# Performance work log

Measured on AMD Instinct MI355X. Metric: run time of the kernel, lower is better.

## Reference

```python
import jax, jax.numpy as jnp
import numpy as np

B = 8192
HID = 1024
VD = 1024
NH = 16
DH = HID // NH  # 64
TOPK = 8
LN_EPS = 1e-5


def setup_inputs() -> dict:
    key = jax.random.key(0)
    ks = jax.random.split(key, 10)
    s = 1.0 / np.sqrt(HID)
    return {
        "hidden_state": jax.random.normal(ks[0], (B, HID), dtype=jnp.float32),
        "memory_keys": jax.random.normal(ks[1], (B, TOPK, HID), dtype=jnp.float32),
        "memory_values": jax.random.normal(ks[2], (B, TOPK, VD), dtype=jnp.float32),
        "Wq": jax.random.normal(ks[3], (HID, HID), dtype=jnp.float32) * s,
        "Wk": jax.random.normal(ks[4], (HID, HID), dtype=jnp.float32) * s,
        "Wv": jax.random.normal(ks[5], (VD, HID), dtype=jnp.float32) * s,
        "Wo": jax.random.normal(ks[6], (HID, HID), dtype=jnp.float32) * s,
        "Wg": jax.random.normal(ks[7], (2 * HID, HID), dtype=jnp.float32) * s,
        "bg": jnp.zeros((HID,), dtype=jnp.float32),
        "ln_g": jnp.ones((HID,), dtype=jnp.float32),
        "ln_b": jnp.zeros((HID,), dtype=jnp.float32),
    }


def reference(hidden_state, memory_keys, memory_values, Wq, Wk, Wv, Wo, Wg, bg, ln_g, ln_b):
    b = hidden_state.shape[0]
    scale = DH ** -0.5
    # QKV projections, reshaped into heads
    Q = (hidden_state @ Wq).reshape(b, NH, DH)          # (B, H, D)
    K = (memory_keys @ Wk).reshape(b, TOPK, NH, DH)     # (B, K, H, D)
    V = (memory_values @ Wv).reshape(b, TOPK, NH, DH)   # (B, K, H, D)
    # attention over top_k memory slots (query length 1)
    scores = jnp.einsum("bhd,bkhd->bhk", Q, K) * scale  # (B, H, K)
    attn = jax.nn.softmax(scores, axis=-1)
    out = jnp.einsum("bhk,bkhd->bhd", attn, V).reshape(b, HID)
    memory_out = out @ Wo
    # gated residual
    gate_in = jnp.concatenate([hidden_state, memory_out], axis=-1)
    g = jax.nn.sigmoid(gate_in @ Wg + bg)
    aug = hidden_state + g * memory_out
    # LayerNorm (affine, eps=1e-5)
    mean = jnp.mean(aug, axis=-1, keepdims=True)
    var = jnp.var(aug, axis=-1, keepdims=True)
    return (aug - mean) * jax.lax.rsqrt(var + LN_EPS) * ln_g + ln_b
```

## Files before the change

kernel.cpp:

```cpp
#include <hip/hip_runtime.h>
#include <hip/hip_bf16.h>

typedef __bf16 bf16;
typedef __bf16 bf16x8 __attribute__((ext_vector_type(8)));
typedef __bf16 bf16x4 __attribute__((ext_vector_type(4)));
typedef float  f32x4  __attribute__((ext_vector_type(4)));

__device__ __forceinline__ void block_barrier()
{
    asm volatile("s_waitcnt lgkmcnt(0)\n\ts_barrier" ::: "memory");
}

#if defined(__has_builtin)
#if __has_builtin(__builtin_amdgcn_global_load_lds)
#define HAS_GLD 1
#endif
#endif
#ifndef HAS_GLD
#define HAS_GLD 0
#endif

__device__ __forceinline__ void gld_lds16(const bf16* g, bf16* lds_base)
{
#if HAS_GLD
    __builtin_amdgcn_global_load_lds(
        (const __attribute__((address_space(1))) void*)g,
        (__attribute__((address_space(3))) void*)lds_base, 16, 0, 0);
#else
    *(bf16x8*)(lds_base + (threadIdx.x & 63) * 8) = *(const bf16x8*)g;
#endif
}

__global__ __launch_bounds__(256)
void transpose_cvt(const float* __restrict__ src, bf16* __restrict__ dst, int K, int N)
{
    __shared__ float t[32][33];
    const int bx = blockIdx.x, by = blockIdx.y, tid = threadIdx.x;
    const int c = tid & 31, r0 = tid >> 5;
#pragma unroll
    for (int p = 0; p < 4; p++) {
        int r = r0 + p * 8;
        t[r][c] = src[(size_t)(by * 32 + r) * N + bx * 32 + c];
    }
    __syncthreads();
#pragma unroll
    for (int p = 0; p < 4; p++) {
        int r = r0 + p * 8;
        dst[(size_t)(bx * 32 + r) * K + by * 32 + c] = (bf16)t[c][r];
    }
}

__global__ __launch_bounds__(256)
void cvt_bf16(const float* __restrict__ src, bf16* __restrict__ dst, int n8)
{
    const int i = blockIdx.x * 256 + threadIdx.x;
    if (i >= n8) return;
    const float4* s = (const float4*)(src + (size_t)i * 8);
    float4 a = s[0], b = s[1];
    bf16x8 o;
    o[0] = (bf16)a.x; o[1] = (bf16)a.y; o[2] = (bf16)a.z; o[3] = (bf16)a.w;
    o[4] = (bf16)b.x; o[5] = (bf16)b.y; o[6] = (bf16)b.z; o[7] = (bf16)b.w;
    *(bf16x8*)(dst + (size_t)i * 8) = o;
}

__global__ __launch_bounds__(256)
void repack_wv(const bf16* __restrict__ Wvt, bf16* __restrict__ Wvf)
{
    const int t = blockIdx.x * 256 + threadIdx.x;
    const int lane = t & 63, g = t >> 6;
    const int dt = g & 3, sp = (g >> 2) & 31, h = g >> 7;
    const int lm = lane & 15, q = lane >> 4;
    const bf16x8 v = *(const bf16x8*)(Wvt + (size_t)(h * 64 + dt * 16 + lm) * 1024
                                      + sp * 32 + q * 8);
    *(bf16x8*)(Wvf + (size_t)g * 512 + lane * 8) = v;
}

template<bool TWOA>
__global__ __launch_bounds__(256)
void gemm_a97(const bf16* __restrict__ A1, const bf16* __restrict__ A2,
              const bf16* __restrict__ Bt, float* __restrict__ Cf,
              bf16* __restrict__ Cb, int Kloop, int Ksplit,
              int ldA, int ldA2, int ldB, int ldC,
              long az, long bz, long cz)
{
    __shared__ bf16 Al[128 * 32];
    __shared__ bf16 Bl[128 * 32];

    const int z = blockIdx.z;
    A1 += (size_t)z * az;
    Bt += (size_t)z * bz;
    if (Cf) Cf += (size_t)z * cz;
    if (Cb) Cb += (size_t)z * cz;

    int bx, by;
    {
        const int gy = gridDim.y;
        const int flat = blockIdx.y * gridDim.x + blockIdx.x;
        if ((gy & 7) == 0 && gridDim.x == 8) {
            const int xcd = flat & 7, slot = flat >> 3, mpx = gy >> 3;
            by = xcd * mpx + (slot >> 3);
            bx = slot & 7;
        } else { bx = blockIdx.x; by = blockIdx.y; }
    }

    const int tid = threadIdx.x;
    const int wave = tid >> 6, lane = tid & 63;
    const int m0 = by * 128, n0 = bx * 128;
    const int rl = lane >> 2;
    const int kc = (lane & 3) * 8;
    const int wm = wave >> 1, wn = wave & 1, lm = lane & 15, quad = lane >> 4;

    f32x4 acc[4][4];
#pragma unroll
    for (int i = 0; i < 4; i++)
#pragma unroll
        for (int j = 0; j < 4; j++)
#pragma unroll
            for (int r = 0; r < 4; r++) acc[i][j][r] = 0.f;

    for (int k0 = 0; k0 < Kloop; k0 += 32) {
        const bf16* Ab; int kof, ld;
        if (TWOA && k0 >= Ksplit) { Ab = A2; kof = k0 - Ksplit; ld = ldA2; }
        else                      { Ab = A1; kof = k0;          ld = ldA;  }
        const int r0 = wave * 32 + rl, r1 = r0 + 16;
        gld_lds16(Ab + (size_t)(m0 + r0) * ld + kof + kc, Al + (wave * 32) * 32);
        gld_lds16(Ab + (size_t)(m0 + r1) * ld + kof + kc, Al + (wave * 32 + 16) * 32);
        gld_lds16(Bt + (size_t)(n0 + r0) * ldB + k0 + kc, Bl + (wave * 32) * 32);
        gld_lds16(Bt + (size_t)(n0 + r1) * ldB + k0 + kc, Bl + (wave * 32 + 16) * 32);
        __syncthreads();

        bf16x8 af[4], bfr[4];
#pragma unroll
        for (int i = 0; i < 4; i++)
            af[i] = *(const bf16x8*)&Al[(wm * 64 + i * 16 + lm) * 32 + quad * 8];
#pragma unroll
        for (int j = 0; j < 4; j++)
            bfr[j] = *(const bf16x8*)&Bl[(wn * 64 + j * 16 + lm) * 32 + quad * 8];
#pragma unroll
        for (int i = 0; i < 4; i++)
#pragma unroll
            for (int j = 0; j < 4; j++)
                acc[i][j] = __builtin_amdgcn_mfma_f32_16x16x32_bf16(af[i], bfr[j], acc[i][j], 0, 0, 0);
        __syncthreads();
    }

#pragma unroll
    for (int i = 0; i < 4; i++) {
        const int rbase = m0 + wm * 64 + i * 16 + quad * 4;
#pragma unroll
        for (int j = 0; j < 4; j++) {
            const int c = n0 + wn * 64 + j * 16 + lm;
#pragma unroll
            for (int r = 0; r < 4; r++) {
                const float v = acc[i][j][r];
                const size_t idx = (size_t)(rbase + r) * ldC + c;
                if (Cf) Cf[idx] = v;
                if (Cb) Cb[idx] = (bf16)v;
            }
        }
    }
}

__global__ __launch_bounds__(512, 4)
void score_attn_part(const bf16* __restrict__ Qb, const bf16* __restrict__ Wkb,
                     const float* __restrict__ mk, float* __restrict__ part)
{
    __shared__ bf16 Ul[16 * 1024];

    const int tid  = threadIdx.x;
    const int wave = tid >> 6, lane = tid & 63;
    const int lm = lane & 15, q = lane >> 4;
    const int g  = blockIdx.x;
    const int c  = blockIdx.y;
    const int i0 = c * 64;
    const int h0 = wave * 2;

    bf16x8 wk[2][4][2];
#pragma unroll
    for (int hh = 0; hh < 2; hh++)
#pragma unroll
        for (int mt = 0; mt < 4; mt++) {
            const bf16* wp = Wkb + (size_t)(i0 + mt * 16 + lm) * 1024 + (h0 + hh) * 64 + q * 8;
            wk[hh][mt][0] = *(const bf16x8*)(wp);
            wk[hh][mt][1] = *(const bf16x8*)(wp + 32);
        }

    float* pbase = part + ((size_t)c << 20);

    for (int t = 0; t < 8; ++t) {
        const int b0 = g * 128 + t * 16;

        bf16x8 qf[2][2];
#pragma unroll
        for (int hh = 0; hh < 2; hh++) {
            const bf16* qp = Qb + (size_t)(b0 + lm) * 1024 + (h0 + hh) * 64 + q * 8;
            qf[hh][0] = *(const bf16x8*)(qp);
            qf[hh][1] = *(const bf16x8*)(qp + 32);
        }

#pragma unroll
        for (int hh = 0; hh < 2; hh++) {
            const int h = h0 + hh;
#pragma unroll
            for (int mt = 0; mt < 4; mt++) {
                f32x4 c4;
                c4[0] = 0.f; c4[1] = 0.f; c4[2] = 0.f; c4[3] = 0.f;
                c4 = __builtin_amdgcn_mfma_f32_16x16x32_bf16(wk[hh][mt][0], qf[hh][0], c4, 0, 0, 0);
                c4 = __builtin_amdgcn_mfma_f32_16x16x32_bf16(wk[hh][mt][1], qf[hh][1], c4, 0, 0, 0);
                bf16x4 o;
                o[0] = (bf16)c4[0]; o[1] = (bf16)c4[1]; o[2] = (bf16)c4[2]; o[3] = (bf16)c4[3];
                *(bf16x4*)((char*)Ul + ((((lm * 16 + h) * 64 + mt * 16 + q * 4) * 2)
                                        ^ (((lm ^ h) & 7) << 4))) = o;
            }
        }
        __syncthreads();

#pragma unroll
        for (int lb = 0; lb < 2; lb++) {
            const int bb = wave * 2 + lb;
            const float* mp = mk + (size_t)(b0 + bb) * 8192 + (lm & 7) * 1024 + i0 + q * 8;
            const f32x4 a0 = *(const f32x4*)(mp);
            const f32x4 a1 = *(const f32x4*)(mp + 4);
            const f32x4 b0v = *(const f32x4*)(mp + 32);
            const f32x4 b1v = *(const f32x4*)(mp + 36);
            bf16x8 m0, m1;
            m0[0] = (bf16)a0[0]; m0[1] = (bf16)a0[1]; m0[2] = (bf16)a0[2]; m0[3] = (bf16)a0[3];
            m0[4] = (bf16)a1[0]; m0[5] = (bf16)a1[1]; m0[6] = (bf16)a1[2]; m0[7] = (bf16)a1[3];
            m1[0] = (bf16)b0v[0]; m1[1] = (bf16)b0v[1]; m1[2] = (bf16)b0v[2]; m1[3] = (bf16)b0v[3];
            m1[4] = (bf16)b1v[0]; m1[5] = (bf16)b1v[1]; m1[6] = (bf16)b1v[2]; m1[7] = (bf16)b1v[3];

            const bf16x8 ua0 = *(const bf16x8*)((char*)Ul +
                ((((bb * 16 + lm) * 64 + q * 8) * 2) ^ (((bb ^ lm) & 7) << 4)));
            const bf16x8 ua1 = *(const bf16x8*)((char*)Ul +
                ((((bb * 16 + lm) * 64 + 32 + q * 8) * 2) ^ (((bb ^ lm) & 7) << 4)));

            f32x4 s4;
            s4[0] = 0.f; s4[1] = 0.f; s4[2] = 0.f; s4[3] = 0.f;
            s4 = __builtin_amdgcn_mfma_f32_16x16x32_bf16(ua0, m0, s4, 0, 0, 0);
            s4 = __builtin_amdgcn_mfma_f32_16x16x32_bf16(ua1, m1, s4, 0, 0, 0);

            if (lm < 8) {
                float* pp = pbase + (size_t)(b0 + bb) * 128 + lm;
#pragma unroll
                for (int r = 0; r < 4; r++) pp[(q * 4 + r) * 8] = s4[r];
            }
        }
        __syncthreads();
    }
}

__global__ __launch_bounds__(256)
void reduce_softmax(const float* __restrict__ part, float* __restrict__ attn)
{
    const int t = blockIdx.x * 256 + threadIdx.x;
    const float* p = part + (size_t)t * 8;
    float s[8] = {0.f, 0.f, 0.f, 0.f, 0.f, 0.f, 0.f, 0.f};
#pragma unroll
    for (int c = 0; c < 16; ++c) {
        const f32x4 a = *(const f32x4*)(p + ((size_t)c << 20));
        const f32x4 b = *(const f32x4*)(p + ((size_t)c << 20) + 4);
        s[0] += a[0]; s[1] += a[1]; s[2] += a[2]; s[3] += a[3];
        s[4] += b[0]; s[5] += b[1]; s[6] += b[2]; s[7] += b[3];
    }
#pragma unroll
    for (int k = 0; k < 8; k++) s[k] *= 0.125f;
    float mx = s[0];
#pragma unroll
    for (int k = 1; k < 8; k++) mx = fmaxf(mx, s[k]);
    float den = 0.f;
#pragma unroll
    for (int k = 0; k < 8; k++) { s[k] = __expf(s[k] - mx); den += s[k]; }
    const float inv = 1.f / den;
    f32x4 o0, o1;
    o0[0] = s[0] * inv; o0[1] = s[1] * inv; o0[2] = s[2] * inv; o0[3] = s[3] * inv;
    o1[0] = s[4] * inv; o1[1] = s[5] * inv; o1[2] = s[6] * inv; o1[3] = s[7] * inv;
    *(f32x4*)(attn + (size_t)t * 8)     = o0;
    *(f32x4*)(attn + (size_t)t * 8 + 4) = o1;
}

__global__ __launch_bounds__(512, 4)
void apply_attn(const float* __restrict__ attn, const float* __restrict__ mv,
                const bf16* __restrict__ Wvf, bf16* __restrict__ OH)
{
    __shared__ float Vl32[3][4096];
    __shared__ bf16  Wl[16 * 16 * 32];

    const int tid  = threadIdx.x;
    const int wave = tid >> 6, lane = tid & 63;
    const int lm = lane & 15, q = lane >> 4;
    const int b0 = blockIdx.x * 16;
    const int h0 = wave * 2;

    const int gk = lane >> 3, gi4 = (lane & 7) * 4;

    bf16x8 afv[2][2];
#pragma unroll
    for (int lb = 0; lb < 2; lb++) {
        const float* ap = attn + (size_t)(b0 + wave * 2 + lb) * 128 + lm * 8;
        const float4 x = *(const float4*)(ap);
        const float4 y = *(const float4*)(ap + 4);
        bf16 a8[8];
        a8[0] = (bf16)x.x; a8[1] = (bf16)x.y; a8[2] = (bf16)x.z; a8[3] = (bf16)x.w;
        a8[4] = (bf16)y.x; a8[5] = (bf16)y.y; a8[6] = (bf16)y.z; a8[7] = (bf16)y.w;
#pragma unroll
        for (int mt = 0; mt < 2; mt++) {
            bf16x8 t;
#pragma unroll
            for (int j = 0; j < 8; j++) t[j] = (q == mt) ? a8[j] : (bf16)0.f;
            afv[lb][mt] = t;
        }
    }

    f32x4 oacc[2][4];
#pragma unroll
    for (int i = 0; i < 2; i++)
#pragma unroll
        for (int j = 0; j < 4; j++)
#pragma unroll
            for (int r = 0; r < 4; r++) oacc[i][j][r] = 0.f;

#pragma unroll
    for (int m = 0; m < 2; m++) {
        const int row = 2 * wave + m;
        gld_lds16((const bf16*)(mv + (size_t)(b0 + row) * 8192 + gk * 1024 + gi4),
                  (bf16*)&Vl32[0][row * 256]);
    }
#pragma unroll
    for (int m = 0; m < 2; m++) {
        const int row = 2 * wave + m;
        gld_lds16((const bf16*)(mv + (size_t)(b0 + row) * 8192 + gk * 1024 + 32 + gi4),
                  (bf16*)&Vl32[1][row * 256]);
    }

    for (int sp = 0; sp < 32; ++sp) {
        const int ni = (sp + 2 < 32) ? sp * 32 + 64 : 0;
        const int cb = sp % 3, nb = (sp + 2) % 3;

        bf16x8 wb[2][4];
#pragma unroll
        for (int hh = 0; hh < 2; hh++) {
            const int h = h0 + hh;
#pragma unroll
            for (int dt = 0; dt < 4; dt++)
                wb[hh][dt] = *(const bf16x8*)(Wvf +
                    ((((size_t)h * 32 + sp) * 4 + dt) * 512 + lane * 8));
        }
        __builtin_amdgcn_sched_barrier(0);

#pragma unroll
        for (int m = 0; m < 2; m++) {
            const int row = 2 * wave + m;
            gld_lds16((const bf16*)(mv + (size_t)(b0 + row) * 8192 + gk * 1024 + ni + gi4),
                      (bf16*)&Vl32[nb][row * 256]);
        }
        __builtin_amdgcn_sched_barrier(0);

        asm volatile("s_waitcnt vmcnt(12)" ::: "memory");
        __builtin_amdgcn_sched_barrier(0);
#pragma unroll
        for (int lb = 0; lb < 2; lb++) {
            const int row = 2 * wave + lb;
            const int il = (q & 1) * 16 + lm;
            float v[8];
#pragma unroll
            for (int k = 0; k < 8; k++) v[k] = Vl32[cb][row * 256 + k * 32 + il];
            bf16x8 avf;
#pragma unroll
            for (int k = 0; k < 8; k++) avf[k] = (bf16)v[k];
#pragma unroll
            for (int mt = 0; mt < 2; mt++) {
                f32x4 c;
                c[0] = 0.f; c[1] = 0.f; c[2] = 0.f; c[3] = 0.f;
                c = __builtin_amdgcn_mfma_f32_16x16x32_bf16(avf, afv[lb][mt], c, 0, 0, 0);
                bf16x4 o;
                o[0] = (bf16)c[0]; o[1] = (bf16)c[1]; o[2] = (bf16)c[2]; o[3] = (bf16)c[3];
                *(bf16x4*)((char*)Wl + ((((row * 16 + lm) * 32 + mt * 16 + q * 4) * 2)
                                        ^ (((row ^ lm) & 7) << 4))) = o;
            }
        }
        block_barrier();

        asm volatile("s_waitcnt vmcnt(2)" ::: "memory");
        __builtin_amdgcn_sched_barrier(0);
#pragma unroll
        for (int hh = 0; hh < 2; hh++) {
            const int h = h0 + hh;
            const bf16x8 wa = *(const bf16x8*)((char*)Wl +
                ((((lm * 16 + h) * 32 + q * 8) * 2) ^ (((lm ^ h) & 7) << 4)));
#pragma unroll
            for (int dt = 0; dt < 4; dt++)
                oacc[hh][dt] = __builtin_amdgcn_mfma_f32_16x16x32_bf16(wa, wb[hh][dt], oacc[hh][dt], 0, 0, 0);
        }
        block_barrier();
    }

#pragma unroll
    for (int hh = 0; hh < 2; hh++) {
        const int h = h0 + hh;
#pragma unroll
        for (int dt = 0; dt < 4; dt++) {
#pragma unroll
            for (int r = 0; r < 4; r++)
                OH[(size_t)(b0 + q * 4 + r) * 1024 + h * 64 + dt * 16 + lm] = (bf16)oacc[hh][dt][r];
        }
    }
}

__global__ __launch_bounds__(256)
void gate_ln_kernel(const float* __restrict__ hs, const float* __restrict__ mo,
                    const float* __restrict__ z,  const float* __restrict__ bg,
                    const float* __restrict__ lng, const float* __restrict__ lnb,
                    float* __restrict__ out)
{
    __shared__ float s1[4], s2[4];
    const int tid = threadIdx.x;
    const size_t base = (size_t)blockIdx.x * 1024 + tid * 4;

    const float4 h4 = *(const float4*)&hs[base];
    const float4 m4 = *(const float4*)&mo[base];
    const float4 z4 = *(const float4*)&z[base];
    const float4 bg4 = *(const float4*)&bg[tid * 4];

    float a[4];
    {
        const float g0 = 1.f / (1.f + __expf(-(z4.x + bg4.x)));
        const float g1 = 1.f / (1.f + __expf(-(z4.y + bg4.y)));
        const float g2 = 1.f / (1.f + __expf(-(z4.z + bg4.z)));
        const float g3 = 1.f / (1.f + __expf(-(z4.w + bg4.w)));
        a[0] = h4.x + g0 * m4.x;
        a[1] = h4.y + g1 * m4.y;
        a[2] = h4.z + g2 * m4.z;
        a[3] = h4.w + g3 * m4.w;
    }
    float sum = a[0] + a[1] + a[2] + a[3];
    float sq  = a[0]*a[0] + a[1]*a[1] + a[2]*a[2] + a[3]*a[3];
#pragma unroll
    for (int off = 32; off >= 1; off >>= 1) {
        sum += __shfl_xor(sum, off);
        sq  += __shfl_xor(sq,  off);
    }
    const int wave = tid >> 6;
    if ((tid & 63) == 0) { s1[wave] = sum; s2[wave] = sq; }
    __syncthreads();
    const float mean = (s1[0] + s1[1] + s1[2] + s1[3]) * (1.f / 1024.f);
    const float var  = (s2[0] + s2[1] + s2[2] + s2[3]) * (1.f / 1024.f) - mean * mean;
    const float inv  = rsqrtf(var + 1e-5f);

    const float4 g4 = *(const float4*)&lng[tid * 4];
    const float4 b4 = *(const float4*)&lnb[tid * 4];
    float4 o;
    o.x = (a[0] - mean) * inv * g4.x + b4.x;
    o.y = (a[1] - mean) * inv * g4.y + b4.y;
    o.z = (a[2] - mean) * inv * g4.z + b4.z;
    o.w = (a[3] - mean) * inv * g4.w + b4.w;
    *(float4*)&out[base] = o;
}

extern "C" void kernel_launch(void* const* d_in, const int* in_sizes, int n_in,
                              void* d_out, int out_size, void* d_ws, size_t ws_size,
                              hipStream_t stream)
{
    const float* hs  = (const float*)d_in[0];
    const float* mk  = (const float*)d_in[1];
    const float* mv  = (const float*)d_in[2];
    const float* Wq  = (const float*)d_in[3];
    const float* Wk  = (const float*)d_in[4];
    const float* Wv  = (const float*)d_in[5];
    const float* Wo  = (const float*)d_in[6];
    const float* Wg  = (const float*)d_in[7];
    const float* bg  = (const float*)d_in[8];
    const float* lng = (const float*)d_in[9];
    const float* lnb = (const float*)d_in[10];
    float* out = (float*)d_out;

    const int B = 8192;
    const dim3 tb(256);

    char* ws = (char*)d_ws;
    bf16*  Wq_t = (bf16*)(ws);
    bf16*  Wv_t = (bf16*)(ws + ((size_t)2  << 20));
    bf16*  Wo_t = (bf16*)(ws + ((size_t)4  << 20));
    bf16*  Wg_t = (bf16*)(ws + ((size_t)6  << 20));
    bf16*  Wk_b = (bf16*)(ws + ((size_t)10 << 20));
    bf16*  hs_b = (bf16*)(ws + ((size_t)12 << 20));
    bf16*  Qb   = (bf16*)(ws + ((size_t)28 << 20));
    bf16*  OH   = (bf16*)(ws + ((size_t)44 << 20));
    float* Mo   = (float*)(ws + ((size_t)60 << 20));
    bf16*  Mo_b = (bf16*)(ws + ((size_t)92 << 20));
    float* Zb   = (float*)(ws + ((size_t)108 << 20));
    float* At   = (float*)(ws + ((size_t)140 << 20));
    float* Atp  = (float*)(ws + ((size_t)144 << 20));
    bf16*  Wvf  = (bf16*)(ws + ((size_t)208 << 20));

    transpose_cvt<<<dim3(32, 32), tb, 0, stream>>>(Wq, Wq_t, 1024, 1024);
    transpose_cvt<<<dim3(32, 32), tb, 0, stream>>>(Wv, Wv_t, 1024, 1024);
    transpose_cvt<<<dim3(32, 32), tb, 0, stream>>>(Wo, Wo_t, 1024, 1024);
    transpose_cvt<<<dim3(32, 64), tb, 0, stream>>>(Wg, Wg_t, 2048, 1024);
    cvt_bf16<<<dim3(1024 * 1024 / 8 / 256), tb, 0, stream>>>(Wk, Wk_b, 1024 * 1024 / 8);
    cvt_bf16<<<dim3(B * 1024 / 8 / 256), tb, 0, stream>>>(hs, hs_b, B * 1024 / 8);
    repack_wv<<<dim3(512), tb, 0, stream>>>(Wv_t, Wvf);

    gemm_a97<false><<<dim3(8, 64, 1), tb, 0, stream>>>(
        hs_b, nullptr, Wq_t, nullptr, Qb,
        1024, 1024, 1024, 0, 1024, 1024, 0, 0, 0);
    score_attn_part<<<dim3(64, 16), dim3(512), 0, stream>>>(Qb, Wk_b, mk, Atp);
    reduce_softmax<<<dim3(512), tb, 0, stream>>>(Atp, At);
    apply_attn<<<dim3(B / 16), dim3(512), 0, stream>>>(At, mv, Wvf, OH);
    gemm_a97<false><<<dim3(8, 64, 1), tb, 0, stream>>>(
        OH, nullptr, Wo_t, Mo, Mo_b,
        1024, 1024, 1024, 0, 1024, 1024, 0, 0, 0);
    gemm_a97<true><<<dim3(8, 64, 1), tb, 0, stream>>>(
        hs_b, Mo_b, Wg_t, Zb, nullptr,
        2048, 1024, 1024, 1024, 2048, 1024, 0, 0, 0);
    gate_ln_kernel<<<dim3(B), tb, 0, stream>>>(
        hs, Mo, Zb, bg, lng, lnb, out);
}
```

Measured before the change: 436.6 us.

## Prefetch memory keys into LDS and repack Q/Wk into fragment layout

score_attn_part now streams the next tile's fp32 memory_keys into LDS via direct global-to-LDS loads while the current tile computes, and prefetches the next Q fragments into registers. New repack_q and repack_wk kernels lay out Q and Wk in MFMA-fragment order so each lane does one contiguous 16-byte load. The goal is to hide global load latency and get coalesced fragment loads. The cost is an extra repack pass over Q (16 MB of bf16), 32 KB more LDS per block, which may reduce occupancy, and extra launches.

```diff
diff --git a/kernel.cpp b/kernel.cpp
--- a/kernel.cpp
+++ b/kernel.cpp
@@ -73,6 +73,30 @@
     const bf16x8 v = *(const bf16x8*)(Wvt + (size_t)(h * 64 + dt * 16 + lm) * 1024
                                       + sp * 32 + q * 8);
     *(bf16x8*)(Wvf + (size_t)g * 512 + lane * 8) = v;
+}
+
+__global__ __launch_bounds__(256)
+void repack_q(const bf16* __restrict__ Qb, bf16* __restrict__ Qf)
+{
+    const int t = blockIdx.x * 256 + threadIdx.x;
+    const int lane = t & 63, g = t >> 6;
+    const int half = g & 1, h = (g >> 1) & 15, bt = g >> 5;
+    const int lm = lane & 15, q = lane >> 4;
+    const bf16x8 v = *(const bf16x8*)(Qb + (size_t)(bt * 16 + lm) * 1024
+                                      + h * 64 + half * 32 + q * 8);
+    *(bf16x8*)(Qf + (size_t)g * 512 + lane * 8) = v;
+}
+
+__global__ __launch_bounds__(256)
+void repack_wk(const bf16* __restrict__ Wkb, bf16* __restrict__ Wkf)
+{
+    const int t = blockIdx.x * 256 + threadIdx.x;
+    const int lane = t & 63, g = t >> 6;
+    const int half = g & 1, mt = (g >> 1) & 3, h = (g >> 3) & 15, c = g >> 7;
+    const int lm = lane & 15, q = lane >> 4;
+    const bf16x8 v = *(const bf16x8*)(Wkb + (size_t)(c * 64 + mt * 16 + lm) * 1024
+                                      + h * 64 + half * 32 + q * 8);
+    *(bf16x8*)(Wkf + (size_t)g * 512 + lane * 8) = v;
 }
 
 template<bool TWOA>
@@ -162,10 +186,11 @@
 }
 
 __global__ __launch_bounds__(512, 4)
-void score_attn_part(const bf16* __restrict__ Qb, const bf16* __restrict__ Wkb,
+void score_attn_part(const bf16* __restrict__ Qf, const bf16* __restrict__ Wkf,
                      const float* __restrict__ mk, float* __restrict__ part)
 {
-    __shared__ bf16 Ul[16 * 1024];
+    __shared__ bf16  Ul[16 * 1024];
+    __shared__ float Ml[8 * 1024];
 
     const int tid  = threadIdx.x;
     const int wave = tid >> 6, lane = tid & 63;
@@ -179,24 +204,56 @@
 #pragma unroll
     for (int hh = 0; hh < 2; hh++)
 #pragma unroll
-        for (int mt = 0; mt < 4; mt++) {
-            const bf16* wp = Wkb + (size_t)(i0 + mt * 16 + lm) * 1024 + (h0 + hh) * 64 + q * 8;
-            wk[hh][mt][0] = *(const bf16x8*)(wp);
-            wk[hh][mt][1] = *(const bf16x8*)(wp + 32);
-        }
+        for (int mt = 0; mt < 4; mt++)
+#pragma unroll
+            for (int half = 0; half < 2; half++)
+                wk[hh][mt][half] = *(const bf16x8*)(Wkf +
+                    (size_t)((((c * 16 + h0 + hh) * 4 + mt) * 2 + half)) * 512 + lane * 8);
+
+    const int choff = lane >> 4, lli = (lane & 15) * 4;
 
     float* pbase = part + ((size_t)c << 20);
+
+    int bt = g * 8;
+    bf16x8 qf[2][2];
+#pragma unroll
+    for (int hh = 0; hh < 2; hh++)
+#pragma unroll
+        for (int half = 0; half < 2; half++)
+            qf[hh][half] = *(const bf16x8*)(Qf +
+                (size_t)(((bt * 16 + h0 + hh) * 2 + half)) * 512 + lane * 8);
+#pragma unroll
+    for (int s = 0; s < 4; s++) {
+        const int chunk = s * 4 + choff;
+        gld_lds16((const bf16*)(mk + (size_t)(bt * 16 + 2 * wave + (chunk >> 3)) * 8192
+                                + (chunk & 7) * 1024 + i0 + lli),
+                  (bf16*)&Ml[wave * 1024 + s * 256]);
+    }
 
     for (int t = 0; t < 8; ++t) {
         const int b0 = g * 128 + t * 16;
-
-        bf16x8 qf[2][2];
-#pragma unroll
-        for (int hh = 0; hh < 2; hh++) {
-            const bf16* qp = Qb + (size_t)(b0 + lm) * 1024 + (h0 + hh) * 64 + q * 8;
-            qf[hh][0] = *(const bf16x8*)(qp);
-            qf[hh][1] = *(const bf16x8*)(qp + 32);
-        }
+        const int btn = (t < 7) ? bt + 1 : bt;
+
+        asm volatile("s_waitcnt vmcnt(0)" ::: "memory");
+        __builtin_amdgcn_sched_barrier(0);
+
+        bf16x8 mbr[2][2];
+#pragma unroll
+        for (int lb = 0; lb < 2; lb++) {
+            const int base = wave * 1024 + (lb * 8 + (lm & 7)) * 64;
+            const f32x4 a0 = *(const f32x4*)&Ml[base + q * 8];
+            const f32x4 a1 = *(const f32x4*)&Ml[base + q * 8 + 4];
+            const f32x4 b0v = *(const f32x4*)&Ml[base + 32 + q * 8];
+            const f32x4 b1v = *(const f32x4*)&Ml[base + 32 + q * 8 + 4];
+            bf16x8 m0, m1;
+            m0[0] = (bf16)a0[0]; m0[1] = (bf16)a0[1]; m0[2] = (bf16)a0[2]; m0[3] = (bf16)a0[3];
+            m0[4] = (bf16)a1[0]; m0[5] = (bf16)a1[1]; m0[6] = (bf16)a1[2]; m0[7] = (bf16)a1[3];
+            m1[0] = (bf16)b0v[0]; m1[1] = (bf16)b0v[1]; m1[2] = (bf16)b0v[2]; m1[3] = (bf16)b0v[3];
+            m1[4] = (bf16)b1v[0]; m1[5] = (bf16)b1v[1]; m1[6] = (bf16)b1v[2]; m1[7] = (bf16)b1v[3];
+            mbr[lb][0] = m0; mbr[lb][1] = m1;
+        }
+        asm volatile("s_waitcnt lgkmcnt(0)" ::: "memory");
+        __builtin_amdgcn_sched_barrier(0);
 
 #pragma unroll
         for (int hh = 0; hh < 2; hh++) {
@@ -213,22 +270,26 @@
                                         ^ (((lm ^ h) & 7) << 4))) = o;
             }
         }
-        __syncthreads();
+
+#pragma unroll
+        for (int hh = 0; hh < 2; hh++)
+#pragma unroll
+            for (int half = 0; half < 2; half++)
+                qf[hh][half] = *(const bf16x8*)(Qf +
+                    (size_t)(((btn * 16 + h0 + hh) * 2 + half)) * 512 + lane * 8);
+#pragma unroll
+        for (int s = 0; s < 4; s++) {
+            const int chunk = s * 4 + choff;
+            gld_lds16((const bf16*)(mk + (size_t)(btn * 16 + 2 * wave + (chunk >> 3)) * 8192
+                                    + (chunk & 7) * 1024 + i0 + lli),
+                      (bf16*)&Ml[wave * 1024 + s * 256]);
+        }
+
+        block_barrier();
 
 #pragma unroll
         for (int lb = 0; lb < 2; lb++) {
             const int bb = wave * 2 + lb;
-            const float* mp = mk + (size_t)(b0 + bb) * 8192 + (lm & 7) * 1024 + i0 + q * 8;
-            const f32x4 a0 = *(const f32x4*)(mp);
-            const f32x4 a1 = *(const f32x4*)(mp + 4);
-            const f32x4 b0v = *(const f32x4*)(mp + 32);
-            const f32x4 b1v = *(const f32x4*)(mp + 36);
-            bf16x8 m0, m1;
-            m0[0] = (bf16)a0[0]; m0[1] = (bf16)a0[1]; m0[2] = (bf16)a0[2]; m0[3] = (bf16)a0[3];
-            m0[4] = (bf16)a1[0]; m0[5] = (bf16)a1[1]; m0[6] = (bf16)a1[2]; m0[7] = (bf16)a1[3];
-            m1[0] = (bf16)b0v[0]; m1[1] = (bf16)b0v[1]; m1[2] = (bf16)b0v[2]; m1[3] = (bf16)b0v[3];
-            m1[4] = (bf16)b1v[0]; m1[5] = (bf16)b1v[1]; m1[6] = (bf16)b1v[2]; m1[7] = (bf16)b1v[3];
-
             const bf16x8 ua0 = *(const bf16x8*)((char*)Ul +
                 ((((bb * 16 + lm) * 64 + q * 8) * 2) ^ (((bb ^ lm) & 7) << 4)));
             const bf16x8 ua1 = *(const bf16x8*)((char*)Ul +
@@ -236,8 +297,8 @@
 
             f32x4 s4;
             s4[0] = 0.f; s4[1] = 0.f; s4[2] = 0.f; s4[3] = 0.f;
-            s4 = __builtin_amdgcn_mfma_f32_16x16x32_bf16(ua0, m0, s4, 0, 0, 0);
-            s4 = __builtin_amdgcn_mfma_f32_16x16x32_bf16(ua1, m1, s4, 0, 0, 0);
+            s4 = __builtin_amdgcn_mfma_f32_16x16x32_bf16(ua0, mbr[lb][0], s4, 0, 0, 0);
+            s4 = __builtin_amdgcn_mfma_f32_16x16x32_bf16(ua1, mbr[lb][1], s4, 0, 0, 0);
 
             if (lm < 8) {
                 float* pp = pbase + (size_t)(b0 + bb) * 128 + lm;
@@ -245,7 +306,9 @@
                 for (int r = 0; r < 4; r++) pp[(q * 4 + r) * 8] = s4[r];
             }
         }
-        __syncthreads();
+        block_barrier();
+
+        bt = btn;
     }
 }
 
@@ -491,6 +554,8 @@
     float* At   = (float*)(ws + ((size_t)140 << 20));
     float* Atp  = (float*)(ws + ((size_t)144 << 20));
     bf16*  Wvf  = (bf16*)(ws + ((size_t)208 << 20));
+    bf16*  Wkf  = (bf16*)(ws + ((size_t)210 << 20));
+    bf16*  Qf   = (bf16*)(ws + ((size_t)212 << 20));
 
     transpose_cvt<<<dim3(32, 32), tb, 0, stream>>>(Wq, Wq_t, 1024, 1024);
     transpose_cvt<<<dim3(32, 32), tb, 0, stream>>>(Wv, Wv_t, 1024, 1024);
@@ -499,11 +564,13 @@
     cvt_bf16<<<dim3(1024 * 1024 / 8 / 256), tb, 0, stream>>>(Wk, Wk_b, 1024 * 1024 / 8);
     cvt_bf16<<<dim3(B * 1024 / 8 / 256), tb, 0, stream>>>(hs, hs_b, B * 1024 / 8);
     repack_wv<<<dim3(512), tb, 0, stream>>>(Wv_t, Wvf);
+    repack_wk<<<dim3(512), tb, 0, stream>>>(Wk_b, Wkf);
 
     gemm_a97<false><<<dim3(8, 64, 1), tb, 0, stream>>>(
         hs_b, nullptr, Wq_t, nullptr, Qb,
         1024, 1024, 1024, 0, 1024, 1024, 0, 0, 0);
-    score_attn_part<<<dim3(64, 16), dim3(512), 0, stream>>>(Qb, Wk_b, mk, Atp);
+    repack_q<<<dim3(4096), tb, 0, stream>>>(Qb, Qf);
+    score_attn_part<<<dim3(64, 16), dim3(512), 0, stream>>>(Qf, Wkf, mk, Atp);
     reduce_softmax<<<dim3(512), tb, 0, stream>>>(Atp, At);
     apply_attn<<<dim3(B / 16), dim3(512), 0, stream>>>(At, mv, Wvf, OH);
     gemm_a97<false><<<dim3(8, 64, 1), tb, 0, stream>>>(
```

New measurement: 452.4 us. 3.6% more time.
